# Performance work log

Hardware: AMD Instinct MI355X
Metric: run time of the kernel (lower is better)

## Reference

```python
import jax, jax.numpy as jnp
import numpy as np

B = 262144
D = 128          # state_dim
L = 8            # levels
STOP_THRESHOLD = 0.6
LN_EPS = 1e-5


def setup_inputs() -> dict:
    key = jax.random.key(0)
    ks = jax.random.split(key, 4)
    signal = jax.random.normal(ks[0], (B, D), dtype=jnp.float32)
    previous = jax.random.normal(ks[1], (B, D), dtype=jnp.float32)
    # nn.Linear default init: U(-1/sqrt(fan_in), 1/sqrt(fan_in)), fan_in = 2D
    bound = 1.0 / np.sqrt(2 * D)
    Wp = jax.random.uniform(ks[2], (L, 2 * D, D), jnp.float32, -bound, bound)  # projection weight (in, out)
    bp = jax.random.uniform(ks[3], (L, D), jnp.float32, -bound, bound)
    # _reset_parameters: gate weight zeros, gate bias -1.2; stop head all zeros
    Wg = jnp.zeros((L, 2 * D, D), jnp.float32)
    bg = jnp.full((L, D), -1.2, jnp.float32)
    Ws = jnp.zeros((L, 2 * D, 1), jnp.float32)
    bs = jnp.zeros((L, 1), jnp.float32)
    gamma = jnp.ones((L, D), jnp.float32)   # LayerNorm weight
    beta = jnp.zeros((L, D), jnp.float32)   # LayerNorm bias
    return {"signal": signal, "previous": previous, "Wp": Wp, "bp": bp,
            "Wg": Wg, "bg": bg, "Ws": Ws, "bs": bs, "gamma": gamma, "beta": beta}


def _layernorm(x, gamma, beta):
    mu = jnp.mean(x, axis=-1, keepdims=True)
    var = jnp.mean(jnp.square(x - mu), axis=-1, keepdims=True)
    return (x - mu) * jax.lax.rsqrt(var + LN_EPS) * gamma + beta


def reference(signal, previous, Wp, bp, Wg, bg, Ws, bs, gamma, beta):
    levels = jnp.arange(1, L + 1, dtype=signal.dtype)

    def step(carry, xs):
        current, acc, active, depth, smass = carry
        Wp_l, bp_l, Wg_l, bg_l, Ws_l, bs_l, g_l, b_l, lvl = xs
        joined = jnp.concatenate([current, previous], axis=-1)           # [B, 2D]
        gate = jax.nn.sigmoid(joined @ Wg_l + bg_l)                      # [B, D]
        candidate = jnp.tanh(joined @ Wp_l + bp_l)                       # [B, D]
        updated = _layernorm(current + gate * (candidate - current), g_l, b_l)
        joined2 = jnp.concatenate([updated, previous], axis=-1)
        adequacy = jax.nn.sigmoid(joined2 @ Ws_l + bs_l)                 # [B, 1]
        stop_prob = jax.nn.sigmoid((adequacy - STOP_THRESHOLD) * 10.0)
        stop_mass = active * stop_prob
        acc = acc + stop_mass * updated
        active = active * (1.0 - stop_prob)
        depth = depth + stop_mass * lvl
        smass = smass + stop_mass
        stats = (jnp.mean(gate, axis=-1),                                # gate mean  [B]
                 jnp.linalg.norm(updated - current, axis=-1),            # delta norm [B]
                 adequacy[:, 0])                                         # adequacy   [B]
        return (updated, acc, active, depth, smass), stats

    init = (signal,
            jnp.zeros_like(signal),
            jnp.ones((signal.shape[0], 1), signal.dtype),
            jnp.zeros((signal.shape[0], 1), signal.dtype),
            jnp.zeros((signal.shape[0], 1), signal.dtype))
    (current, acc, active, depth, smass), (gates, deltas, adeqs) = jax.lax.scan(
        step, init, (Wp, bp, Wg, bg, Ws, bs, gamma, beta, levels))

    accumulated = acc + active * current
    stop_depth = depth + active * float(L)
    gate_mean = jnp.mean(gates, axis=0)       # mean over levels -> [B]
    delta_mean = jnp.mean(deltas, axis=0)
    adequacy_mean = jnp.mean(adeqs, axis=0)
    return (accumulated, gate_mean, delta_mean,
            stop_depth[:, 0], smass[:, 0], adequacy_mean)
```

## Files before the change

### kernel.cpp

```cpp
#include <hip/hip_runtime.h>
#include <math.h>

#define NB 262144
#define ND 128
#define NL 8

typedef __bf16 bf16x8 __attribute__((ext_vector_type(8)));
typedef float  f32x4  __attribute__((ext_vector_type(4)));

union BFP { unsigned int u; __bf16 h[2]; unsigned short s[2]; };
union F4  { float4 f; float a[4]; };

__device__ __forceinline__ float sigm(float x){ return 1.0f/(1.0f + __expf(-x)); }
__device__ __forceinline__ float tanhfast(float x){
  float t = __expf(-2.0f*fabsf(x));
  return copysignf((1.0f - t)/(1.0f + t), x);
}
__device__ __forceinline__ float redrow(float v){
  v += __shfl_xor(v, 16);
  v += __shfl_xor(v, 32);
  return v;
}
__device__ __forceinline__ unsigned int pk2(float a, float b){
  BFP x; x.h[0]=(__bf16)a; x.h[1]=(__bf16)b; return x.u;
}
__device__ __forceinline__ float ubf(unsigned int u, int hi){
  BFP x; x.u = u; return (float)x.h[hi];
}
__device__ __forceinline__ void gload16(const void* g, void* s){
  __builtin_amdgcn_global_load_lds((const __attribute__((address_space(1))) unsigned int*)g,
                                   (__attribute__((address_space(3))) unsigned int*)s,
                                   16, 0, 0);
}

__global__ void repack_w(const float* __restrict__ Wp, const float* __restrict__ Wg,
                         uint4* __restrict__ dst){
  int t = blockIdx.x*256 + threadIdx.x;
  int lane = t & 63;
  int frag = t >> 6;
  int cf = frag & 7, kf = (frag >> 3) & 7, mat = (frag >> 6) & 1, l = frag >> 7;
  const float* W = mat ? Wp : Wg;
  int k = kf*32 + (lane >> 4)*8;
  int n = cf*16 + (lane & 15);
  const float* src = W + (l*256 + k)*ND + n;
  bf16x8 v;
#pragma unroll
  for (int j=0;j<8;++j) v[j] = (__bf16)src[j*ND];
  dst[((l*2 + mat)*64 + kf*8 + cf)*64 + lane] = __builtin_bit_cast(uint4, v);
}

__global__ void prevdot_k(const float* __restrict__ previous, const float* __restrict__ Ws,
                          const float* __restrict__ bs, float* __restrict__ pdot){
  int t = blockIdx.x*256 + threadIdx.x;
  int row = t >> 4, g = t & 15;
  const float* p = previous + (size_t)row*ND + g*8;
  float4 a = *(const float4*)p;
  float4 b = *(const float4*)(p+4);
#pragma unroll
  for (int l=0;l<NL;++l){
    const float* w = Ws + l*256 + 128 + g*8;
    float s = a.x*w[0] + a.y*w[1] + a.z*w[2] + a.w*w[3]
            + b.x*w[4] + b.y*w[5] + b.z*w[6] + b.w*w[7];
    s += __shfl_xor(s,1); s += __shfl_xor(s,2); s += __shfl_xor(s,4); s += __shfl_xor(s,8);
    if (g==0) pdot[row*NL + l] = s + bs[l];
  }
}

__global__ __attribute__((amdgpu_flat_work_group_size(256,256)))
           __attribute__((amdgpu_waves_per_eu(2,2)))
void fused_k(const float* __restrict__ signal, const float* __restrict__ previous,
             const float* __restrict__ bp, const float* __restrict__ bg,
             const float* __restrict__ Ws, const float* __restrict__ gamma,
             const float* __restrict__ beta,
             const uint4* __restrict__ wpk, const float* __restrict__ pdot,
             float* __restrict__ out)
{
  __shared__ unsigned short tile[128*256];
  __shared__ uint4 wbuf[2][512];

  const int tid  = threadIdx.x;
  const int w    = tid >> 6;
  const int lane = tid & 63;
  const int llo  = lane & 15;
  const int lhi  = lane >> 4;
  const int rbase = w * 32;
  const int row0  = blockIdx.x * 128;
  const int swz   = (llo & 7) << 4;

  auto gstage = [&](int s, int b){
    const char* src = (const char*)wpk + (size_t)s*8192;
    char* d = (char*)&wbuf[b][0];
    gload16(src + tid*16, d + tid*16);
    gload16(src + 4096 + tid*16, d + 4096 + tid*16);
  };

  gstage(0, 0);

  unsigned int gstash[2][16];
  float accv[2][8][4];
  f32x4 pacc[2][8];
  float active[2], depth[2], smass[2], gsum[2], dsum[2], asum[2];

#pragma unroll
  for (int g=0; g<2; ++g){
    int rl = rbase + g*16 + llo;
    int rowg = row0 + rl;
#pragma unroll
    for (int cf=0; cf<8; ++cf){
      F4 v; v.f = *(const float4*)&signal[(size_t)rowg*ND + 16*cf + 4*lhi];
      unsigned p0 = pk2(v.a[0], v.a[1]);
      unsigned p1 = pk2(v.a[2], v.a[3]);
      char* dst = (char*)tile + rl*512 + ((32*cf + 8*lhi) ^ swz);
      *(unsigned long long*)dst = (unsigned long long)p0 | ((unsigned long long)p1 << 32);
      pacc[g][cf] = (f32x4){0.f,0.f,0.f,0.f};
#pragma unroll
      for (int j=0;j<4;++j) accv[g][cf][j] = 0.f;
    }
#pragma unroll
    for (int kfp=0; kfp<4; ++kfp){
      const float* p = previous + (size_t)rowg*ND + kfp*32 + lhi*8;
      F4 a; a.f = *(const float4*)p;
      F4 b; b.f = *(const float4*)(p+4);
      uint4 pv;
      pv.x = pk2(a.a[0], a.a[1]);
      pv.y = pk2(a.a[2], a.a[3]);
      pv.z = pk2(b.a[0], b.a[1]);
      pv.w = pk2(b.a[2], b.a[3]);
      char* dst = (char*)tile + rl*512 + ((256 + 64*kfp + 16*lhi) ^ swz);
      *(uint4*)dst = pv;
    }
    active[g]=1.f; depth[g]=0.f; smass[g]=0.f; gsum[g]=0.f; dsum[g]=0.f; asum[g]=0.f;
  }

  auto compute = [&](int s){
    int kf  = s & 7;
    int buf = s & 1;
    int off = (64*kf + 16*lhi) ^ swz;
    const char* tb = (const char*)tile;
    bf16x8 xf0 = __builtin_bit_cast(bf16x8, *(const uint4*)(tb + (rbase      + llo)*512 + off));
    bf16x8 xf1 = __builtin_bit_cast(bf16x8, *(const uint4*)(tb + (rbase + 16 + llo)*512 + off));
    const uint4* wb = &wbuf[buf][lane];
#pragma unroll
    for (int cf=0; cf<8; ++cf){
      bf16x8 wf = __builtin_bit_cast(bf16x8, wb[cf*64]);
      pacc[0][cf] = __builtin_amdgcn_mfma_f32_16x16x32_bf16(wf, xf0, pacc[0][cf], 0,0,0);
      pacc[1][cf] = __builtin_amdgcn_mfma_f32_16x16x32_bf16(wf, xf1, pacc[1][cf], 0,0,0);
    }
  };

  auto gate_epi = [&](int lev){
#pragma unroll
    for (int g=0; g<2; ++g){
      float gp = 0.f;
#pragma unroll
      for (int cf=0; cf<8; ++cf){
        F4 bgv; bgv.f = *(const float4*)&bg[lev*ND + 16*cf + 4*lhi];
        float g0 = sigm(pacc[g][cf][0] + bgv.a[0]);
        float g1 = sigm(pacc[g][cf][1] + bgv.a[1]);
        float g2 = sigm(pacc[g][cf][2] + bgv.a[2]);
        float g3 = sigm(pacc[g][cf][3] + bgv.a[3]);
        gp += g0 + g1 + g2 + g3;
        gstash[g][2*cf]   = pk2(g0, g1);
        gstash[g][2*cf+1] = pk2(g2, g3);
        pacc[g][cf] = (f32x4){0.f,0.f,0.f,0.f};
      }
      gsum[g] += redrow(gp) * (1.0f/ND);
    }
  };

  auto cand_epi = [&](int lev, bool wrtile){
#pragma unroll
    for (int g=0; g<2; ++g){
      int rl = rbase + g*16 + llo;
      int rowg = row0 + rl;
      const char* cbase = (const char*)tile + rl*512;
      float s1 = 0.f, s2 = 0.f;
#pragma unroll
      for (int cf=0; cf<8; ++cf){
        F4 bpv; bpv.f = *(const float4*)&bp[lev*ND + 16*cf + 4*lhi];
        unsigned long long cw = *(const unsigned long long*)(cbase + ((32*cf + 8*lhi) ^ swz));
        unsigned c0 = (unsigned)cw, c1 = (unsigned)(cw >> 32);
#pragma unroll
        for (int j=0;j<4;++j){
          float cand = tanhfast(pacc[g][cf][j] + bpv.a[j]);
          float c  = ubf(j<2 ? c0 : c1, j&1);
          float gt = ubf(gstash[g][2*cf + (j>>1)], j&1);
          float x = c + gt*(cand - c);
          pacc[g][cf][j] = x;
          s1 += x; s2 += x*x;
        }
      }
      s1 = redrow(s1); s2 = redrow(s2);
      float mu  = s1*(1.0f/ND);
      float inv = rsqrtf(s2*(1.0f/ND) - mu*mu + 1e-5f);
      float dp = 0.f, ap = 0.f;
#pragma unroll
      for (int cf=0; cf<8; ++cf){
        F4 gm; gm.f = *(const float4*)&gamma[lev*ND + 16*cf + 4*lhi];
        F4 bt; bt.f = *(const float4*)&beta [lev*ND + 16*cf + 4*lhi];
        F4 wv; wv.f = *(const float4*)&Ws   [lev*2*ND + 16*cf + 4*lhi];
        unsigned long long cw = *(const unsigned long long*)(cbase + ((32*cf + 8*lhi) ^ swz));
        unsigned c0 = (unsigned)cw, c1 = (unsigned)(cw >> 32);
#pragma unroll
        for (int j=0;j<4;++j){
          float un = (pacc[g][cf][j] - mu)*inv*gm.a[j] + bt.a[j];
          float c  = ubf(j<2 ? c0 : c1, j&1);
          float df = un - c;
          dp += df*df;
          ap += un*wv.a[j];
          pacc[g][cf][j] = un;
        }
      }
      dp = redrow(dp); ap = redrow(ap);
      float adq = sigm(ap + pdot[(size_t)rowg*NL + lev]);
      float sp  = sigm((adq - 0.6f)*10.0f);
      float sm  = active[g]*sp;
      asum[g] += adq;
      dsum[g] += sqrtf(dp);
      depth[g] += sm * (float)(lev+1);
      smass[g] += sm;
      active[g] *= (1.0f - sp);
#pragma unroll
      for (int cf=0; cf<8; ++cf){
#pragma unroll
        for (int j=0;j<4;++j) accv[g][cf][j] += sm * pacc[g][cf][j];
        if (wrtile){
          unsigned p0 = pk2(pacc[g][cf][0], pacc[g][cf][1]);
          unsigned p1 = pk2(pacc[g][cf][2], pacc[g][cf][3]);
          char* dst = (char*)tile + rl*512 + ((32*cf + 8*lhi) ^ swz);
          *(unsigned long long*)dst = (unsigned long long)p0 | ((unsigned long long)p1 << 32);
          pacc[g][cf] = (f32x4){0.f,0.f,0.f,0.f};
        }
      }
    }
    if (wrtile){
      asm volatile("s_waitcnt lgkmcnt(0)" ::: "memory");
      __builtin_amdgcn_sched_barrier(0);
    }
  };

#pragma unroll 1
  for (int l=0; l<NL; ++l){
#pragma unroll 1
    for (int q=0; q<16; ++q){
      int s = l*16 + q;
      __syncthreads();
      if (s+1 < 128) gstage(s+1, (s+1)&1);
      if (q == 8) gate_epi(l);
      if (q == 0 && l > 0) cand_epi(l-1, true);
      compute(s);
    }
  }
  cand_epi(NL-1, false);

#pragma unroll
  for (int g=0; g<2; ++g){
    int rowg = row0 + rbase + g*16 + llo;
#pragma unroll
    for (int cf=0; cf<8; ++cf){
      F4 o;
#pragma unroll
      for (int j=0;j<4;++j)
        o.a[j] = accv[g][cf][j] + active[g]*pacc[g][cf][j];
      *(float4*)&out[(size_t)rowg*ND + 16*cf + 4*lhi] = o.f;
    }
  }
  if (lhi == 0){
    const size_t BD = (size_t)NB*ND;
#pragma unroll
    for (int g=0; g<2; ++g){
      int rowg = row0 + rbase + g*16 + llo;
      out[BD + rowg]                = gsum[g]*(1.0f/NL);
      out[BD + NB + rowg]           = dsum[g]*(1.0f/NL);
      out[BD + 2*(size_t)NB + rowg] = depth[g] + active[g]*(float)NL;
      out[BD + 3*(size_t)NB + rowg] = smass[g];
      out[BD + 4*(size_t)NB + rowg] = asum[g]*(1.0f/NL);
    }
  }
}

extern "C" void kernel_launch(void* const* d_in, const int* in_sizes, int n_in,
                              void* d_out, int out_size, void* d_ws, size_t ws_size,
                              hipStream_t stream){
  const float* signal   = (const float*)d_in[0];
  const float* previous = (const float*)d_in[1];
  const float* Wp    = (const float*)d_in[2];
  const float* bp    = (const float*)d_in[3];
  const float* Wg    = (const float*)d_in[4];
  const float* bg    = (const float*)d_in[5];
  const float* Ws    = (const float*)d_in[6];
  const float* bs    = (const float*)d_in[7];
  const float* gamma = (const float*)d_in[8];
  const float* beta  = (const float*)d_in[9];

  uint4* wpk  = (uint4*)d_ws;
  float* pdot = (float*)((char*)d_ws + (size_t)NL*2*65536);

  repack_w<<<256, 256, 0, stream>>>(Wp, Wg, wpk);
  prevdot_k<<<NB/16, 256, 0, stream>>>(previous, Ws, bs, pdot);
  fused_k<<<NB/128, 256, 0, stream>>>(signal, previous, bp, bg, Ws, gamma, beta,
                                      wpk, pdot, (float*)d_out);
}
```

Baseline: 1.061 ms.

## Split each 128-row block across eight waves with sixteen rows per wave

The fused kernel moves from 256 threads (4 waves, 32 rows each) to 512 threads (8 waves, 16 rows each) per 128-row block. Each wave keeps half the accumulators and stash registers, and the weight staging per step is now one 16-byte load per thread. The intent is lower register pressure and more waves to hide MFMA, epilogue and barrier latency. In exchange, each weight fragment read from LDS is reused by only one MFMA instead of two, and the per-step __syncthreads now spans twice as many waves.

```diff
diff --git a/kernel.cpp b/kernel.cpp
--- a/kernel.cpp
+++ b/kernel.cpp
@@ -66,8 +66,7 @@
   }
 }
 
-__global__ __attribute__((amdgpu_flat_work_group_size(256,256)))
-           __attribute__((amdgpu_waves_per_eu(2,2)))
+__global__ __launch_bounds__(512)
 void fused_k(const float* __restrict__ signal, const float* __restrict__ previous,
              const float* __restrict__ bp, const float* __restrict__ bg,
              const float* __restrict__ Ws, const float* __restrict__ gamma,
@@ -83,27 +82,22 @@
   const int lane = tid & 63;
   const int llo  = lane & 15;
   const int lhi  = lane >> 4;
-  const int rbase = w * 32;
+  const int rbase = w * 16;
   const int row0  = blockIdx.x * 128;
   const int swz   = (llo & 7) << 4;
 
   auto gstage = [&](int s, int b){
-    const char* src = (const char*)wpk + (size_t)s*8192;
-    char* d = (char*)&wbuf[b][0];
-    gload16(src + tid*16, d + tid*16);
-    gload16(src + 4096 + tid*16, d + 4096 + tid*16);
-  };
-
+    gload16((const char*)wpk + (size_t)s*8192 + tid*16, (char*)&wbuf[b][0] + tid*16);
+  };
   gstage(0, 0);
 
-  unsigned int gstash[2][16];
-  float accv[2][8][4];
-  f32x4 pacc[2][8];
-  float active[2], depth[2], smass[2], gsum[2], dsum[2], asum[2];
-
-#pragma unroll
-  for (int g=0; g<2; ++g){
-    int rl = rbase + g*16 + llo;
+  unsigned int gstash[16];
+  float accv[8][4];
+  f32x4 pacc[8];
+  float active, depth, smass, gsum, dsum, asum;
+
+  {
+    int rl = rbase + llo;
     int rowg = row0 + rl;
 #pragma unroll
     for (int cf=0; cf<8; ++cf){
@@ -112,9 +106,9 @@
       unsigned p1 = pk2(v.a[2], v.a[3]);
       char* dst = (char*)tile + rl*512 + ((32*cf + 8*lhi) ^ swz);
       *(unsigned long long*)dst = (unsigned long long)p0 | ((unsigned long long)p1 << 32);
-      pacc[g][cf] = (f32x4){0.f,0.f,0.f,0.f};
-#pragma unroll
-      for (int j=0;j<4;++j) accv[g][cf][j] = 0.f;
+      pacc[cf] = (f32x4){0.f,0.f,0.f,0.f};
+#pragma unroll
+      for (int j=0;j<4;++j) accv[cf][j] = 0.f;
     }
 #pragma unroll
     for (int kfp=0; kfp<4; ++kfp){
@@ -129,111 +123,103 @@
       char* dst = (char*)tile + rl*512 + ((256 + 64*kfp + 16*lhi) ^ swz);
       *(uint4*)dst = pv;
     }
-    active[g]=1.f; depth[g]=0.f; smass[g]=0.f; gsum[g]=0.f; dsum[g]=0.f; asum[g]=0.f;
+    active=1.f; depth=0.f; smass=0.f; gsum=0.f; dsum=0.f; asum=0.f;
   }
 
   auto compute = [&](int s){
     int kf  = s & 7;
     int buf = s & 1;
     int off = (64*kf + 16*lhi) ^ swz;
-    const char* tb = (const char*)tile;
-    bf16x8 xf0 = __builtin_bit_cast(bf16x8, *(const uint4*)(tb + (rbase      + llo)*512 + off));
-    bf16x8 xf1 = __builtin_bit_cast(bf16x8, *(const uint4*)(tb + (rbase + 16 + llo)*512 + off));
+    bf16x8 xf = __builtin_bit_cast(bf16x8,
+        *(const uint4*)((const char*)tile + (rbase + llo)*512 + off));
     const uint4* wb = &wbuf[buf][lane];
 #pragma unroll
     for (int cf=0; cf<8; ++cf){
       bf16x8 wf = __builtin_bit_cast(bf16x8, wb[cf*64]);
-      pacc[0][cf] = __builtin_amdgcn_mfma_f32_16x16x32_bf16(wf, xf0, pacc[0][cf], 0,0,0);
-      pacc[1][cf] = __builtin_amdgcn_mfma_f32_16x16x32_bf16(wf, xf1, pacc[1][cf], 0,0,0);
+      pacc[cf] = __builtin_amdgcn_mfma_f32_16x16x32_bf16(wf, xf, pacc[cf], 0,0,0);
     }
   };
 
   auto gate_epi = [&](int lev){
-#pragma unroll
-    for (int g=0; g<2; ++g){
-      float gp = 0.f;
-#pragma unroll
-      for (int cf=0; cf<8; ++cf){
-        F4 bgv; bgv.f = *(const float4*)&bg[lev*ND + 16*cf + 4*lhi];
-        float g0 = sigm(pacc[g][cf][0] + bgv.a[0]);
-        float g1 = sigm(pacc[g][cf][1] + bgv.a[1]);
-        float g2 = sigm(pacc[g][cf][2] + bgv.a[2]);
-        float g3 = sigm(pacc[g][cf][3] + bgv.a[3]);
-        gp += g0 + g1 + g2 + g3;
-        gstash[g][2*cf]   = pk2(g0, g1);
-        gstash[g][2*cf+1] = pk2(g2, g3);
-        pacc[g][cf] = (f32x4){0.f,0.f,0.f,0.f};
+    float gp = 0.f;
+#pragma unroll
+    for (int cf=0; cf<8; ++cf){
+      F4 bgv; bgv.f = *(const float4*)&bg[lev*ND + 16*cf + 4*lhi];
+      float g0 = sigm(pacc[cf][0] + bgv.a[0]);
+      float g1 = sigm(pacc[cf][1] + bgv.a[1]);
+      float g2 = sigm(pacc[cf][2] + bgv.a[2]);
+      float g3 = sigm(pacc[cf][3] + bgv.a[3]);
+      gp += g0 + g1 + g2 + g3;
+      gstash[2*cf]   = pk2(g0, g1);
+      gstash[2*cf+1] = pk2(g2, g3);
+      pacc[cf] = (f32x4){0.f,0.f,0.f,0.f};
+    }
+    gsum += redrow(gp) * (1.0f/ND);
+  };
+
+  auto cand_epi = [&](int lev, bool wr){
+    int rl = rbase + llo;
+    int rowg = row0 + rl;
+    char* cbase = (char*)tile + rl*512;
+    float s1 = 0.f, s2 = 0.f;
+#pragma unroll
+    for (int cf=0; cf<8; ++cf){
+      F4 bpv; bpv.f = *(const float4*)&bp[lev*ND + 16*cf + 4*lhi];
+      unsigned long long cw = *(const unsigned long long*)(cbase + ((32*cf + 8*lhi) ^ swz));
+      unsigned c0 = (unsigned)cw, c1 = (unsigned)(cw >> 32);
+#pragma unroll
+      for (int j=0;j<4;++j){
+        float cand = tanhfast(pacc[cf][j] + bpv.a[j]);
+        float cc = ubf(j<2 ? c0 : c1, j&1);
+        float gt = ubf(gstash[2*cf + (j>>1)], j&1);
+        float x = cc + gt*(cand - cc);
+        pacc[cf][j] = x;
+        s1 += x; s2 += x*x;
       }
-      gsum[g] += redrow(gp) * (1.0f/ND);
-    }
-  };
-
-  auto cand_epi = [&](int lev, bool wrtile){
-#pragma unroll
-    for (int g=0; g<2; ++g){
-      int rl = rbase + g*16 + llo;
-      int rowg = row0 + rl;
-      const char* cbase = (const char*)tile + rl*512;
-      float s1 = 0.f, s2 = 0.f;
-#pragma unroll
-      for (int cf=0; cf<8; ++cf){
-        F4 bpv; bpv.f = *(const float4*)&bp[lev*ND + 16*cf + 4*lhi];
-        unsigned long long cw = *(const unsigned long long*)(cbase + ((32*cf + 8*lhi) ^ swz));
-        unsigned c0 = (unsigned)cw, c1 = (unsigned)(cw >> 32);
-#pragma unroll
-        for (int j=0;j<4;++j){
-          float cand = tanhfast(pacc[g][cf][j] + bpv.a[j]);
-          float c  = ubf(j<2 ? c0 : c1, j&1);
-          float gt = ubf(gstash[g][2*cf + (j>>1)], j&1);
-          float x = c + gt*(cand - c);
-          pacc[g][cf][j] = x;
-          s1 += x; s2 += x*x;
-        }
+    }
+    s1 = redrow(s1); s2 = redrow(s2);
+    float mu  = s1*(1.0f/ND);
+    float inv = rsqrtf(s2*(1.0f/ND) - mu*mu + 1e-5f);
+    float dp = 0.f, ap = 0.f;
+#pragma unroll
+    for (int cf=0; cf<8; ++cf){
+      F4 gm; gm.f = *(const float4*)&gamma[lev*ND + 16*cf + 4*lhi];
+      F4 bt; bt.f = *(const float4*)&beta [lev*ND + 16*cf + 4*lhi];
+      F4 wv; wv.f = *(const float4*)&Ws   [lev*2*ND + 16*cf + 4*lhi];
+      unsigned long long cw = *(const unsigned long long*)(cbase + ((32*cf + 8*lhi) ^ swz));
+      unsigned c0 = (unsigned)cw, c1 = (unsigned)(cw >> 32);
+#pragma unroll
+      for (int j=0;j<4;++j){
+        float un = (pacc[cf][j] - mu)*inv*gm.a[j] + bt.a[j];
+        float cc = ubf(j<2 ? c0 : c1, j&1);
+        float df = un - cc;
+        dp += df*df;
+        ap += un*wv.a[j];
+        pacc[cf][j] = un;
       }
-      s1 = redrow(s1); s2 = redrow(s2);
-      float mu  = s1*(1.0f/ND);
-      float inv = rsqrtf(s2*(1.0f/ND) - mu*mu + 1e-5f);
-      float dp = 0.f, ap = 0.f;
-#pragma unroll
-      for (int cf=0; cf<8; ++cf){
-        F4 gm; gm.f = *(const float4*)&gamma[lev*ND + 16*cf + 4*lhi];
-        F4 bt; bt.f = *(const float4*)&beta [lev*ND + 16*cf + 4*lhi];
-        F4 wv; wv.f = *(const float4*)&Ws   [lev*2*ND + 16*cf + 4*lhi];
-        unsigned long long cw = *(const unsigned long long*)(cbase + ((32*cf + 8*lhi) ^ swz));
-        unsigned c0 = (unsigned)cw, c1 = (unsigned)(cw >> 32);
-#pragma unroll
-        for (int j=0;j<4;++j){
-          float un = (pacc[g][cf][j] - mu)*inv*gm.a[j] + bt.a[j];
-          float c  = ubf(j<2 ? c0 : c1, j&1);
-          float df = un - c;
-          dp += df*df;
-          ap += un*wv.a[j];
-          pacc[g][cf][j] = un;
-        }
+    }
+    dp = redrow(dp); ap = redrow(ap);
+    float adq = sigm(ap + pdot[(size_t)rowg*NL + lev]);
+    float sp  = sigm((adq - 0.6f)*10.0f);
+    float sm  = active*sp;
+    asum += adq;
+    dsum += sqrtf(dp);
+    depth += sm * (float)(lev+1);
+    smass += sm;
+    active *= (1.0f - sp);
+#pragma unroll
+    for (int cf=0; cf<8; ++cf){
+#pragma unroll
+      for (int j=0;j<4;++j) accv[cf][j] += sm * pacc[cf][j];
+      if (wr){
+        unsigned p0 = pk2(pacc[cf][0], pacc[cf][1]);
+        unsigned p1 = pk2(pacc[cf][2], pacc[cf][3]);
+        char* dst = cbase + ((32*cf + 8*lhi) ^ swz);
+        *(unsigned long long*)dst = (unsigned long long)p0 | ((unsigned long long)p1 << 32);
+        pacc[cf] = (f32x4){0.f,0.f,0.f,0.f};
       }
-      dp = redrow(dp); ap = redrow(ap);
-      float adq = sigm(ap + pdot[(size_t)rowg*NL + lev]);
-      float sp  = sigm((adq - 0.6f)*10.0f);
-      float sm  = active[g]*sp;
-      asum[g] += adq;
-      dsum[g] += sqrtf(dp);
-      depth[g] += sm * (float)(lev+1);
-      smass[g] += sm;
-      active[g] *= (1.0f - sp);
-#pragma unroll
-      for (int cf=0; cf<8; ++cf){
-#pragma unroll
-        for (int j=0;j<4;++j) accv[g][cf][j] += sm * pacc[g][cf][j];
-        if (wrtile){
-          unsigned p0 = pk2(pacc[g][cf][0], pacc[g][cf][1]);
-          unsigned p1 = pk2(pacc[g][cf][2], pacc[g][cf][3]);
-          char* dst = (char*)tile + rl*512 + ((32*cf + 8*lhi) ^ swz);
-          *(unsigned long long*)dst = (unsigned long long)p0 | ((unsigned long long)p1 << 32);
-          pacc[g][cf] = (f32x4){0.f,0.f,0.f,0.f};
-        }
-      }
-    }
-    if (wrtile){
+    }
+    if (wr){
       asm volatile("s_waitcnt lgkmcnt(0)" ::: "memory");
       __builtin_amdgcn_sched_barrier(0);
     }
@@ -253,28 +239,23 @@
   }
   cand_epi(NL-1, false);
 
-#pragma unroll
-  for (int g=0; g<2; ++g){
-    int rowg = row0 + rbase + g*16 + llo;
+  {
+    int rowg = row0 + rbase + llo;
 #pragma unroll
     for (int cf=0; cf<8; ++cf){
       F4 o;
 #pragma unroll
       for (int j=0;j<4;++j)
-        o.a[j] = accv[g][cf][j] + active[g]*pacc[g][cf][j];
+        o.a[j] = accv[cf][j] + active*pacc[cf][j];
       *(float4*)&out[(size_t)rowg*ND + 16*cf + 4*lhi] = o.f;
     }
-  }
-  if (lhi == 0){
-    const size_t BD = (size_t)NB*ND;
-#pragma unroll
-    for (int g=0; g<2; ++g){
-      int rowg = row0 + rbase + g*16 + llo;
-      out[BD + rowg]                = gsum[g]*(1.0f/NL);
-      out[BD + NB + rowg]           = dsum[g]*(1.0f/NL);
-      out[BD + 2*(size_t)NB + rowg] = depth[g] + active[g]*(float)NL;
-      out[BD + 3*(size_t)NB + rowg] = smass[g];
-      out[BD + 4*(size_t)NB + rowg] = asum[g]*(1.0f/NL);
+    if (lhi == 0){
+      const size_t BD = (size_t)NB*ND;
+      out[BD + rowg]                = gsum*(1.0f/NL);
+      out[BD + NB + rowg]           = dsum*(1.0f/NL);
+      out[BD + 2*(size_t)NB + rowg] = depth + active*(float)NL;
+      out[BD + 3*(size_t)NB + rowg] = smass;
+      out[BD + 4*(size_t)NB + rowg] = asum*(1.0f/NL);
     }
   }
 }
@@ -298,6 +279,6 @@
 
   repack_w<<<256, 256, 0, stream>>>(Wp, Wg, wpk);
   prevdot_k<<<NB/16, 256, 0, stream>>>(previous, Ws, bs, pdot);
-  fused_k<<<NB/128, 256, 0, stream>>>(signal, previous, bp, bg, Ws, gamma, beta,
+  fused_k<<<NB/128, 512, 0, stream>>>(signal, previous, bp, bg, Ws, gamma, beta,
                                       wpk, pdot, (float*)d_out);
 }
```

Result: no change. 1.045 ms (-1.5%).
